# Performance work log

Measured on AMD Instinct MI355X. Metric: run time of the kernel, lower is better.

The kernel has to match this reference:

```python
import jax, jax.numpy as jnp
import numpy as np

N_ATOMS = 4096
HSIZE = 128
N_HEADS = 8
D_K = HSIZE // N_HEADS


def setup_inputs() -> dict:
    key = jax.random.key(0)
    ks = jax.random.split(key, 11)
    s = 1.0 / np.sqrt(HSIZE)
    return {
        "query": jax.random.normal(ks[0], (N_ATOMS, HSIZE), dtype=jnp.float32),
        "key": jax.random.normal(ks[1], (N_ATOMS, HSIZE), dtype=jnp.float32),
        "value": jax.random.normal(ks[2], (N_ATOMS, HSIZE), dtype=jnp.float32),
        "mask": jax.random.randint(ks[3], (N_ATOMS, N_ATOMS), 0, 2, dtype=jnp.int32),
        "Wq": jax.random.normal(ks[4], (HSIZE, HSIZE), dtype=jnp.float32) * s,
        "bq": jnp.zeros((HSIZE,), dtype=jnp.float32),
        "Wk": jax.random.normal(ks[5], (HSIZE, HSIZE), dtype=jnp.float32) * s,
        "bk": jnp.zeros((HSIZE,), dtype=jnp.float32),
        "Wv": jax.random.normal(ks[6], (HSIZE, HSIZE), dtype=jnp.float32) * s,
        "bv": jnp.zeros((HSIZE,), dtype=jnp.float32),
        "Wo": jax.random.normal(ks[7], (HSIZE, HSIZE), dtype=jnp.float32) * s,
    }


def _mha(query, key, value, mask, Wq, bq, Wk, bk, Wv, bv, Wo):
    n = query.shape[0]
    # project and split heads: [n, hsize] -> [H, n, d_k]
    def heads(x, W, b):
        return (x @ W.T + b).reshape(n, N_HEADS, D_K).transpose(1, 0, 2)
    q = heads(query, Wq, bq)
    k = heads(key, Wk, bk)
    v = heads(value, Wv, bv)
    scale = 1.0 / jnp.sqrt(jnp.asarray(D_K, q.dtype))
    scores = jnp.einsum("hnd,hmd->hnm", q, k) * scale  # [H, n, n]
    scores = jnp.where(mask[None, :, :] == 0, jnp.asarray(-1e9, scores.dtype), scores)
    p_attn = jax.nn.softmax(scores, axis=-1)
    x = jnp.einsum("hnm,hmd->hnd", p_attn, v)  # [H, n, d_k]
    x = x.transpose(1, 0, 2).reshape(n, HSIZE)  # merge heads
    return x @ Wo.T  # output_linear has bias=False


def reference(query, key, value, mask, Wq, bq, Wk, bk, Wv, bv, Wo):
    return _mha(query, key, value, mask, Wq, bq, Wk, bk, Wv, bv, Wo)
```

## Files before the change

### kernel.cpp

```cpp
#include <hip/hip_runtime.h>
#include <hip/hip_bf16.h>

#define NA 4096
#define HS 128
#define CSTR 136

typedef unsigned short u16;
typedef unsigned long long u64;
using bf16x8  = __attribute__((ext_vector_type(8))) short;
using f32x4   = __attribute__((ext_vector_type(4))) float;
using ushort8 = __attribute__((ext_vector_type(8))) unsigned short;
using u32x4   = __attribute__((ext_vector_type(4))) unsigned;

#define QSCALE 0.18033688011112042f

static __device__ __forceinline__ u16 f2bf(float f) {
    unsigned u = __builtin_bit_cast(unsigned, f);
    u += 0x7FFFu + ((u >> 16) & 1u);
    return (u16)(u >> 16);
}

static __device__ __forceinline__ unsigned pkbf(float a, float b) {
    float2 f; f.x = a; f.y = b;
    __hip_bfloat162 r = __float22bfloat162_rn(f);
    unsigned u;
    __builtin_memcpy(&u, &r, 4);
    return u;
}

__global__ __launch_bounds__(256) void proj_pack(
    const float* __restrict__ Xq, const float* __restrict__ Xk, const float* __restrict__ Xv,
    const float* __restrict__ Wq, const float* __restrict__ Wk,
    const float* __restrict__ Wv, const float* __restrict__ Wo,
    const float* __restrict__ bq, const float* __restrict__ bk,
    const float* __restrict__ bv,
    u16* __restrict__ Qbh, u16* __restrict__ Kbh, u16* __restrict__ VtB,
    u16* __restrict__ WoF)
{
    const int blk = blockIdx.x;
    const int t = threadIdx.x;

    __shared__ __align__(16) u16 Ws[16384];
    __shared__ __align__(16) u16 Xs[32 * CSTR];
    __shared__ __align__(16) u16 Cs[32 * CSTR];

    if (blk >= 384) {
        const int gid = (blk - 384) * 256 + t;
        const int off = gid * 4;
        float4 v = *(const float4*)(Wo + off);
        ushort4 o;
        o.x = f2bf(v.x); o.y = f2bf(v.y); o.z = f2bf(v.z); o.w = f2bf(v.w);
        const int j = off >> 7, k0 = off & 127;
        const int j0 = j >> 4, c = j & 15, kk = k0 >> 5, q = (k0 >> 3) & 3;
        *(ushort4*)(WoF + ((j0 * 4 + kk) * 16 + c) * 32 + q * 8 + (k0 & 7)) = o;
        return;
    }

    const int pb = blk;
    const int mat = pb >> 7;
    const float* X = (mat == 0) ? Xq : (mat == 1) ? Xk : Xv;
    const float* Wsrc = (mat == 0) ? Wq : (mat == 1) ? Wk : Wv;
    const float* bsrc = (mat == 0) ? bq : (mat == 1) ? bk : bv;
    const float sc = (mat == 0) ? QSCALE : 1.0f;
    const int r0b = (pb & 127) * 32;

    {
        const int base = t * 64;
#pragma unroll
        for (int i = 0; i < 16; ++i) {
            const int off = base + i * 4;
            float4 v = *(const float4*)(Wsrc + off);
            ushort4 o;
            o.x = f2bf(v.x * sc); o.y = f2bf(v.y * sc);
            o.z = f2bf(v.z * sc); o.w = f2bf(v.w * sc);
            const int j = off >> 7, k0 = off & 127;
            const int j0 = j >> 4, c2 = j & 15, kk = k0 >> 5, qq = (k0 >> 3) & 3;
            *(ushort4*)(Ws + (j0 * 4 + kk) * 512 + qq * 128 + c2 * 8 + (k0 & 7)) = o;
        }
    }

    {
        const int r = t >> 3, cb = (t & 7) * 16;
        const float* Xr = X + (size_t)(r0b + r) * HS + cb;
#pragma unroll
        for (int seg = 0; seg < 4; ++seg) {
            float4 f = *(const float4*)(Xr + seg * 4);
            ushort4 u;
            u.x = f2bf(f.x); u.y = f2bf(f.y); u.z = f2bf(f.z); u.w = f2bf(f.w);
            *(ushort4*)(Xs + r * CSTR + cb + seg * 4) = u;
        }
    }
    __syncthreads();

    const int wv = t >> 6, lane = t & 63;
    const int c = lane & 15, q = lane >> 4;
    const int rw = (wv & 1) * 16;
    const int j0b = (wv >> 1) * 4;

    bf16x8 af[4];
#pragma unroll
    for (int kk = 0; kk < 4; ++kk)
        af[kk] = *(const bf16x8*)(Xs + (rw + c) * CSTR + kk * 32 + q * 8);

    const f32x4 zero = {0.f, 0.f, 0.f, 0.f};
#pragma unroll
    for (int jj = 0; jj < 4; ++jj) {
        const int j0 = j0b + jj;
        f32x4 acc = zero;
#pragma unroll
        for (int kk = 0; kk < 4; ++kk) {
            bf16x8 bf = *(const bf16x8*)(Ws + (j0 * 4 + kk) * 512 + q * 128 + c * 8);
            acc = __builtin_amdgcn_mfma_f32_16x16x32_bf16(af[kk], bf, acc, 0, 0, 0);
        }
        const float bias = bsrc[j0 * 16 + c] * sc;
#pragma unroll
        for (int r = 0; r < 4; ++r)
            Cs[(rw + 4 * q + r) * CSTR + j0 * 16 + c] = f2bf(acc[r] + bias);
    }
    __syncthreads();

    if (mat < 2) {
        u16* dst = (mat == 0) ? Qbh : Kbh;
        const int h8 = t >> 5, r = t & 31;
        const u16* src = Cs + r * CSTR + h8 * 16;
        int drow = r0b + r;
        if (mat == 1) {
            const int k = (r0b & 32) + r;
            const int slot = ((k >> 5) * 2 + ((k >> 2) & 1)) * 16
                           + ((k >> 3) & 3) * 4 + (k & 3);
            drow = (r0b & ~63) + slot;
        }
        u16* dp = dst + (size_t)h8 * (NA * 16) + (size_t)drow * 16;
        *(bf16x8*)(dp)     = *(const bf16x8*)(src);
        *(bf16x8*)(dp + 8) = *(const bf16x8*)(src + 8);
    } else {
        const int d = t >> 1, s = t & 1;
        const int kb = r0b >> 6, ko = (r0b & 32) + s * 16;
        ushort8 v0, v1;
#pragma unroll
        for (int jj = 0; jj < 8; ++jj) v0[jj] = Cs[(s * 16 + jj) * CSTR + d];
#pragma unroll
        for (int jj = 0; jj < 8; ++jj) v1[jj] = Cs[(s * 16 + 8 + jj) * CSTR + d];
        u16* dp = VtB + (size_t)kb * 8192 + d * 64 + ko;
        *(ushort8*)(dp)     = v0;
        *(ushort8*)(dp + 8) = v1;
    }
}

__global__ __launch_bounds__(512, 4) void attn(
    const int* __restrict__ mask,
    const u16* __restrict__ Qbh, const u16* __restrict__ Kbh, const u16* __restrict__ VtB,
    float* __restrict__ part)
{
    __shared__ __align__(8)  u64 Mwp[16 * 17];
    __shared__ __align__(8)  u64 Mtab[16];
    __shared__ __align__(16) unsigned char Msc[8 * 512];

    const int t = threadIdx.x;
    const int h = t >> 6;
    const int lane = t & 63;
    const int c = lane & 15;
    const int q = lane >> 4;
    const int tile = blockIdx.x, split = blockIdx.y;
    const int i0 = tile * 16;
    const int kt0 = split * 1024;

    {
#pragma unroll
        for (int rr = 0; rr < 2; ++rr) {
            const int row = h * 2 + rr;
            const int* mrow = mask + (size_t)(i0 + row) * NA + kt0;
            unsigned char* dst = Msc + h * 512 + rr * 256;
#pragma unroll
            for (int ch = 0; ch < 4; ++ch) {
                const int4 v = *(const int4*)(mrow + ch * 256 + lane * 4);
                const unsigned nib = (v.x != 0 ? 1u : 0u) | (v.y != 0 ? 2u : 0u)
                                   | (v.z != 0 ? 4u : 0u) | (v.w != 0 ? 8u : 0u);
                dst[ch * 64 + lane] = (unsigned char)nib;
            }
        }
        if (lane < 32) {
            const int rr = lane >> 4, k = lane & 15;
            const int row = h * 2 + rr;
            const uint4 b16 = *(const uint4*)(Msc + h * 512 + rr * 256 + k * 16);
            unsigned z[4];
            const unsigned xs4[4] = { b16.x, b16.y, b16.z, b16.w };
#pragma unroll
            for (int i = 0; i < 4; ++i) {
                unsigned x = xs4[i];
                x = (x | (x >> 4)) & 0x00FF00FFu;
                x = (x | (x >> 8)) & 0x0000FFFFu;
                z[i] = x;
            }
            Mwp[row * 17 + k] = (u64)(z[0] | (z[1] << 16))
                              | ((u64)(z[2] | (z[3] << 16)) << 32);
        }
    }
    if (t < 16) {
        const unsigned lo = ((t & 1) ? 0xFFFFu : 0u) | ((t & 2) ? 0xFFFF0000u : 0u);
        const unsigned hi = ((t & 4) ? 0xFFFFu : 0u) | ((t & 8) ? 0xFFFF0000u : 0u);
        Mtab[t] = (u64)lo | ((u64)hi << 32);
    }

    const u16* Qh = Qbh + (size_t)h * (NA * 16);
    const u16* Kh = Kbh + (size_t)h * (NA * 16);

    const bf16x8 qf = *(const bf16x8*)(Qh + (size_t)(i0 + c) * 16 + (q & 1) * 8);

    bf16x8 ones;
#pragma unroll
    for (int i = 0; i < 8; ++i) ones[i] = (short)0x3F80;

    __syncthreads();

    const f32x4 zero = {0.f, 0.f, 0.f, 0.f};
    f32x4 Oacc = zero;
    f32x4 Lacc = zero;

    bf16x8 kf[4];
#pragma unroll
    for (int t4 = 0; t4 < 4; ++t4)
        kf[t4] = *(const bf16x8*)(Kh + (size_t)(kt0 + t4 * 16 + c) * 16 + (q & 1) * 8);

#pragma unroll 1
    for (int it = 0; it < 16; ++it) {
        const int kt = kt0 + it * 64;
        const u16* Vb = VtB + (size_t)(kt >> 6) * 8192 + (h * 16 + c) * 64;

        bf16x8 vf0 = *(const bf16x8*)(Vb + q * 8);
        bf16x8 vf1 = *(const bf16x8*)(Vb + 32 + q * 8);

        f32x4 ST[4];
        __builtin_amdgcn_s_setprio(1);
#pragma unroll
        for (int t4 = 0; t4 < 4; ++t4)
            ST[t4] = __builtin_amdgcn_mfma_f32_16x16x32_bf16(kf[t4], qf, zero, 0, 0, 0);
        __builtin_amdgcn_s_setprio(0);

        const int ktn = kt0 + ((it + 1) & 15) * 64;
#pragma unroll
        for (int t4 = 0; t4 < 4; ++t4)
            kf[t4] = *(const bf16x8*)(Kh + (size_t)(ktn + t4 * 16 + c) * 16 + (q & 1) * 8);

        const u64 w = Mwp[c * 17 + it];
        const unsigned wa = (unsigned)(w >> (8 * q));
        const unsigned wb = (unsigned)(w >> (32 + 8 * q));

        unsigned pl[4], ph[4];
#pragma unroll
        for (int t4 = 0; t4 < 4; ++t4) {
            const unsigned nib = (((t4 & 2) ? wb : wa) >> ((t4 & 1) * 4)) & 15u;
            float p0 = __builtin_amdgcn_exp2f(ST[t4][0]);
            float p1 = __builtin_amdgcn_exp2f(ST[t4][1]);
            float p2 = __builtin_amdgcn_exp2f(ST[t4][2]);
            float p3 = __builtin_amdgcn_exp2f(ST[t4][3]);
            const unsigned lo = pkbf(p0, p1);
            const unsigned hi = pkbf(p2, p3);
            const u64 mex = Mtab[nib];
            pl[t4] = lo & (unsigned)mex;
            ph[t4] = hi & (unsigned)(mex >> 32);
        }
        const u32x4 a0 = { pl[0], ph[0], pl[1], ph[1] };
        const u32x4 a1 = { pl[2], ph[2], pl[3], ph[3] };
        const bf16x8 pf0 = __builtin_bit_cast(bf16x8, a0);
        const bf16x8 pf1 = __builtin_bit_cast(bf16x8, a1);

        __builtin_amdgcn_s_setprio(1);
        Oacc = __builtin_amdgcn_mfma_f32_16x16x32_bf16(pf0, vf0, Oacc, 0, 0, 0);
        Oacc = __builtin_amdgcn_mfma_f32_16x16x32_bf16(pf1, vf1, Oacc, 0, 0, 0);
        Lacc = __builtin_amdgcn_mfma_f32_16x16x32_bf16(pf0, ones, Lacc, 0, 0, 0);
        Lacc = __builtin_amdgcn_mfma_f32_16x16x32_bf16(pf1, ones, Lacc, 0, 0, 0);
        __builtin_amdgcn_s_setprio(0);
    }

    float* base = part + (size_t)((tile * 4 + split) * 8 + h) * 272;
#pragma unroll
    for (int r = 0; r < 4; ++r)
        base[(4 * q + r) * 16 + c] = Oacc[r];
    if (c == 0) {
#pragma unroll
        for (int r = 0; r < 4; ++r)
            base[256 + 4 * q + r] = Lacc[r];
    }
}

__global__ __launch_bounds__(256) void reduce_out(
    const float* __restrict__ part, const u16* __restrict__ WoF,
    float* __restrict__ out)
{
    __shared__ __align__(16) u16 xs[16 * CSTR];

    const int t = threadIdx.x;
    const int tile = blockIdx.x;
    const int i0 = tile * 16;
    const float* Pt = part + (size_t)tile * 4 * 8 * 272;

    {
        const int i = t >> 4, d = t & 15;
#pragma unroll
        for (int h = 0; h < 8; ++h) {
            float os = 0.f, ls = 0.f;
#pragma unroll
            for (int s = 0; s < 4; ++s) {
                const float* b = Pt + (size_t)(s * 8 + h) * 272;
                os += b[i * 16 + d];
                ls += b[256 + i];
            }
            xs[i * CSTR + h * 16 + d] = f2bf(os / ls);
        }
    }
    __syncthreads();

    const int wv = t >> 6, lane = t & 63;
    const int c = lane & 15, q = lane >> 4;

    bf16x8 af[4];
#pragma unroll
    for (int kk = 0; kk < 4; ++kk)
        af[kk] = *(const bf16x8*)(xs + c * CSTR + kk * 32 + q * 8);

    const f32x4 zero = {0.f, 0.f, 0.f, 0.f};
#pragma unroll
    for (int jj = 0; jj < 2; ++jj) {
        const int j0 = wv * 2 + jj;
        f32x4 acc = zero;
#pragma unroll
        for (int kk = 0; kk < 4; ++kk) {
            bf16x8 bf = *(const bf16x8*)(WoF + (j0 * 4 + kk) * 512 + c * 32 + q * 8);
            acc = __builtin_amdgcn_mfma_f32_16x16x32_bf16(af[kk], bf, acc, 0, 0, 0);
        }
#pragma unroll
        for (int r = 0; r < 4; ++r)
            out[(size_t)(i0 + 4 * q + r) * HS + j0 * 16 + c] = acc[r];
    }
}

extern "C" void kernel_launch(void* const* d_in, const int* in_sizes, int n_in,
                              void* d_out, int out_size, void* d_ws, size_t ws_size,
                              hipStream_t stream) {
    const float* query = (const float*)d_in[0];
    const float* key   = (const float*)d_in[1];
    const float* value = (const float*)d_in[2];
    const int*   mask  = (const int*)d_in[3];
    const float* Wq    = (const float*)d_in[4];
    const float* bq    = (const float*)d_in[5];
    const float* Wk    = (const float*)d_in[6];
    const float* bk    = (const float*)d_in[7];
    const float* Wv    = (const float*)d_in[8];
    const float* bv    = (const float*)d_in[9];
    const float* Wo    = (const float*)d_in[10];

    u16* Qbh = (u16*)d_ws;
    u16* Kbh = Qbh + (size_t)NA * HS;
    u16* VtB = Kbh + (size_t)NA * HS;
    u16* WoF = VtB + (size_t)NA * HS;
    float* partb = (float*)(WoF + 16384);

    proj_pack<<<400, 256, 0, stream>>>(query, key, value, Wq, Wk, Wv, Wo,
                                       bq, bk, bv, Qbh, Kbh, VtB, WoF);
    attn<<<dim3(256, 4), 512, 0, stream>>>(mask, Qbh, Kbh, VtB, partb);
    reduce_out<<<256, 256, 0, stream>>>(partb, WoF, (float*)d_out);
}
```

Measured before the change: 168.1 us.

## Split mask preprocessing in halves and overlap second half with attention loop

The mask bitpacking for the block's 1024-key split is now done in two halves. The first half is packed before the loop. The second half's global loads are issued into registers up front and packed into shared memory after the first eight iterations, followed by a barrier. This is meant to hide mask-load latency behind the first half of the attention compute. In exchange it holds extra registers live across the loop and adds a barrier mid-kernel.

```diff
diff --git a/kernel.cpp b/kernel.cpp
--- a/kernel.cpp
+++ b/kernel.cpp
@@ -154,7 +154,7 @@
 {
     __shared__ __align__(8)  u64 Mwp[16 * 17];
     __shared__ __align__(8)  u64 Mtab[16];
-    __shared__ __align__(16) unsigned char Msc[8 * 512];
+    __shared__ __align__(16) unsigned char Msc[8 * 256];
 
     const int t = threadIdx.x;
     const int h = t >> 6;
@@ -168,21 +168,19 @@
     {
 #pragma unroll
         for (int rr = 0; rr < 2; ++rr) {
-            const int row = h * 2 + rr;
-            const int* mrow = mask + (size_t)(i0 + row) * NA + kt0;
-            unsigned char* dst = Msc + h * 512 + rr * 256;
-#pragma unroll
-            for (int ch = 0; ch < 4; ++ch) {
+            const int* mrow = mask + (size_t)(i0 + h * 2 + rr) * NA + kt0;
+            unsigned char* dst = Msc + h * 256 + rr * 128;
+#pragma unroll
+            for (int ch = 0; ch < 2; ++ch) {
                 const int4 v = *(const int4*)(mrow + ch * 256 + lane * 4);
                 const unsigned nib = (v.x != 0 ? 1u : 0u) | (v.y != 0 ? 2u : 0u)
                                    | (v.z != 0 ? 4u : 0u) | (v.w != 0 ? 8u : 0u);
                 dst[ch * 64 + lane] = (unsigned char)nib;
             }
         }
-        if (lane < 32) {
-            const int rr = lane >> 4, k = lane & 15;
-            const int row = h * 2 + rr;
-            const uint4 b16 = *(const uint4*)(Msc + h * 512 + rr * 256 + k * 16);
+        if (lane < 16) {
+            const int rr = lane >> 3, k = lane & 7;
+            const uint4 b16 = *(const uint4*)(Msc + h * 256 + rr * 128 + k * 16);
             unsigned z[4];
             const unsigned xs4[4] = { b16.x, b16.y, b16.z, b16.w };
 #pragma unroll
@@ -192,10 +190,19 @@
                 x = (x | (x >> 8)) & 0x0000FFFFu;
                 z[i] = x;
             }
-            Mwp[row * 17 + k] = (u64)(z[0] | (z[1] << 16))
-                              | ((u64)(z[2] | (z[3] << 16)) << 32);
-        }
-    }
+            Mwp[(h * 2 + rr) * 17 + k] = (u64)(z[0] | (z[1] << 16))
+                                       | ((u64)(z[2] | (z[3] << 16)) << 32);
+        }
+    }
+
+    int4 m2[4];
+#pragma unroll
+    for (int rr = 0; rr < 2; ++rr)
+#pragma unroll
+        for (int ch = 0; ch < 2; ++ch)
+            m2[rr * 2 + ch] = *(const int4*)(mask + (size_t)(i0 + h * 2 + rr) * NA
+                                             + kt0 + 512 + ch * 256 + lane * 4);
+
     if (t < 16) {
         const unsigned lo = ((t & 1) ? 0xFFFFu : 0u) | ((t & 2) ? 0xFFFF0000u : 0u);
         const unsigned hi = ((t & 4) ? 0xFFFFu : 0u) | ((t & 8) ? 0xFFFF0000u : 0u);
@@ -223,7 +230,85 @@
         kf[t4] = *(const bf16x8*)(Kh + (size_t)(kt0 + t4 * 16 + c) * 16 + (q & 1) * 8);
 
 #pragma unroll 1
-    for (int it = 0; it < 16; ++it) {
+    for (int it = 0; it < 8; ++it) {
+        const int kt = kt0 + it * 64;
+        const u16* Vb = VtB + (size_t)(kt >> 6) * 8192 + (h * 16 + c) * 64;
+
+        bf16x8 vf0 = *(const bf16x8*)(Vb + q * 8);
+        bf16x8 vf1 = *(const bf16x8*)(Vb + 32 + q * 8);
+
+        f32x4 ST[4];
+        __builtin_amdgcn_s_setprio(1);
+#pragma unroll
+        for (int t4 = 0; t4 < 4; ++t4)
+            ST[t4] = __builtin_amdgcn_mfma_f32_16x16x32_bf16(kf[t4], qf, zero, 0, 0, 0);
+        __builtin_amdgcn_s_setprio(0);
+
+        const int ktn = kt0 + ((it + 1) & 15) * 64;
+#pragma unroll
+        for (int t4 = 0; t4 < 4; ++t4)
+            kf[t4] = *(const bf16x8*)(Kh + (size_t)(ktn + t4 * 16 + c) * 16 + (q & 1) * 8);
+
+        const u64 w = Mwp[c * 17 + it];
+        const unsigned wa = (unsigned)(w >> (8 * q));
+        const unsigned wb = (unsigned)(w >> (32 + 8 * q));
+
+        unsigned pl[4], ph[4];
+#pragma unroll
+        for (int t4 = 0; t4 < 4; ++t4) {
+            const unsigned nib = (((t4 & 2) ? wb : wa) >> ((t4 & 1) * 4)) & 15u;
+            float p0 = __builtin_amdgcn_exp2f(ST[t4][0]);
+            float p1 = __builtin_amdgcn_exp2f(ST[t4][1]);
+            float p2 = __builtin_amdgcn_exp2f(ST[t4][2]);
+            float p3 = __builtin_amdgcn_exp2f(ST[t4][3]);
+            const unsigned lo = pkbf(p0, p1);
+            const unsigned hi = pkbf(p2, p3);
+            const u64 mex = Mtab[nib];
+            pl[t4] = lo & (unsigned)mex;
+            ph[t4] = hi & (unsigned)(mex >> 32);
+        }
+        const u32x4 a0 = { pl[0], ph[0], pl[1], ph[1] };
+        const u32x4 a1 = { pl[2], ph[2], pl[3], ph[3] };
+        const bf16x8 pf0 = __builtin_bit_cast(bf16x8, a0);
+        const bf16x8 pf1 = __builtin_bit_cast(bf16x8, a1);
+
+        __builtin_amdgcn_s_setprio(1);
+        Oacc = __builtin_amdgcn_mfma_f32_16x16x32_bf16(pf0, vf0, Oacc, 0, 0, 0);
+        Oacc = __builtin_amdgcn_mfma_f32_16x16x32_bf16(pf1, vf1, Oacc, 0, 0, 0);
+        Lacc = __builtin_amdgcn_mfma_f32_16x16x32_bf16(pf0, ones, Lacc, 0, 0, 0);
+        Lacc = __builtin_amdgcn_mfma_f32_16x16x32_bf16(pf1, ones, Lacc, 0, 0, 0);
+        __builtin_amdgcn_s_setprio(0);
+    }
+
+    {
+#pragma unroll
+        for (int idx = 0; idx < 4; ++idx) {
+            const int rr = idx >> 1, ch = idx & 1;
+            const int4 v = m2[idx];
+            const unsigned nib = (v.x != 0 ? 1u : 0u) | (v.y != 0 ? 2u : 0u)
+                               | (v.z != 0 ? 4u : 0u) | (v.w != 0 ? 8u : 0u);
+            Msc[h * 256 + rr * 128 + ch * 64 + lane] = (unsigned char)nib;
+        }
+        if (lane < 16) {
+            const int rr = lane >> 3, k = lane & 7;
+            const uint4 b16 = *(const uint4*)(Msc + h * 256 + rr * 128 + k * 16);
+            unsigned z[4];
+            const unsigned xs4[4] = { b16.x, b16.y, b16.z, b16.w };
+#pragma unroll
+            for (int i = 0; i < 4; ++i) {
+                unsigned x = xs4[i];
+                x = (x | (x >> 4)) & 0x00FF00FFu;
+                x = (x | (x >> 8)) & 0x0000FFFFu;
+                z[i] = x;
+            }
+            Mwp[(h * 2 + rr) * 17 + 8 + k] = (u64)(z[0] | (z[1] << 16))
+                                           | ((u64)(z[2] | (z[3] << 16)) << 32);
+        }
+    }
+    __syncthreads();
+
+#pragma unroll 1
+    for (int it = 8; it < 16; ++it) {
         const int kt = kt0 + it * 64;
         const u16* Vb = VtB + (size_t)(kt >> 6) * 8192 + (h * 16 + c) * 64;
 
```

After: 170.4 us. No clear change (+1.4%).
